# Kernel tuning notes

Hardware: AMD Instinct MI355X
Metric: run time of the kernel (lower is better)

## Reference

```python
import jax, jax.numpy as jnp
import numpy as np

IN, OUT, IO, CF, CS = 128, 128, 512, 512, 1024
B = 8192
TAU_IO, TAU_CF, TAU_CS = 2.0, 5.0, 70.0


def _lin(x, W, b):
    # torch nn.Linear: y = x @ W.T + b, W has shape [out, in]
    return x @ W.T + b


def setup_inputs() -> dict:
    key = jax.random.key(0)
    ks = jax.random.split(key, 24)

    def wb(i, fan_out, fan_in):
        s = 1.0 / np.sqrt(fan_in)
        W = jax.random.uniform(ks[2 * i], (fan_out, fan_in), jnp.float32, -s, s)
        b = jax.random.uniform(ks[2 * i + 1], (fan_out,), jnp.float32, -s, s)
        return W, b

    Wi2io, bi2io = wb(0, IO, IN)
    Wio2o, bio2o = wb(1, OUT, IO)
    Wio2io, bio2io = wb(2, IO, IO)
    Wio2cf, bio2cf = wb(3, CF, IO)
    Wcf2io, bcf2io = wb(4, IO, CF)
    Wcf2cs, bcf2cs = wb(5, CS, CF)
    Wcf2cf, bcf2cf = wb(6, CF, CF)
    Wcs2cf, bcs2cf = wb(7, CF, CS)
    Wcs2cs, bcs2cs = wb(8, CS, CS)

    x = jax.random.normal(ks[18], (B, IN), jnp.float32)
    io_state = jnp.zeros((B, IO), jnp.float32)
    cf_state = jnp.zeros((B, CF), jnp.float32)
    cs_state = jnp.zeros((B, CS), jnp.float32)

    return dict(
        x=x, io_state=io_state, cf_state=cf_state, cs_state=cs_state,
        Wi2io=Wi2io, bi2io=bi2io, Wio2o=Wio2o, bio2o=bio2o,
        Wio2io=Wio2io, bio2io=bio2io, Wio2cf=Wio2cf, bio2cf=bio2cf,
        Wcf2io=Wcf2io, bcf2io=bcf2io, Wcf2cs=Wcf2cs, bcf2cs=bcf2cs,
        Wcf2cf=Wcf2cf, bcf2cf=bcf2cf, Wcs2cf=Wcs2cf, bcs2cf=bcs2cf,
        Wcs2cs=Wcs2cs, bcs2cs=bcs2cs,
    )


def reference(x, io_state, cf_state, cs_state,
              Wi2io, bi2io, Wio2o, bio2o,
              Wio2io, bio2io, Wio2cf, bio2cf,
              Wcf2io, bcf2io, Wcf2cs, bcf2cs,
              Wcf2cf, bcf2cf, Wcs2cf, bcs2cf,
              Wcs2cs, bcs2cs):
    x = x.reshape(-1, IN)
    # leaky-integrated updates; all branches read the *previous* states
    io_new = jnp.tanh(
        (1.0 - 1.0 / TAU_IO) * io_state
        + (_lin(io_state, Wio2io, bio2io)
           + _lin(cf_state, Wcf2io, bcf2io)
           + _lin(x, Wi2io, bi2io)) / TAU_IO)
    cf_new = jnp.tanh(
        (1.0 - 1.0 / TAU_CF) * cf_state
        + (_lin(cf_state, Wcf2cf, bcf2cf)
           + _lin(cs_state, Wcs2cf, bcs2cf)
           + _lin(io_state, Wio2cf, bio2cf)) / TAU_CF)
    cs_new = jnp.tanh(
        (1.0 - 1.0 / TAU_CS) * cs_state
        + (_lin(cs_state, Wcs2cs, bcs2cs)
           + _lin(cf_state, Wcf2cs, bcf2cs)) / TAU_CS)
    y = jnp.tanh(_lin(io_new, Wio2o, bio2o))
    return y
```

## Files before the change

### kernel.cpp

```cpp
#include <hip/hip_runtime.h>


typedef float f32x4 __attribute__((ext_vector_type(4)));
typedef __bf16 bf16x8 __attribute__((ext_vector_type(8)));
typedef unsigned short u16x8 __attribute__((ext_vector_type(8)));
typedef unsigned short u16x4 __attribute__((ext_vector_type(4)));

__device__ __forceinline__ unsigned short f2bf(float f) {
    unsigned u = __builtin_bit_cast(unsigned, f);
    u += 0x7FFFu + ((u >> 16) & 1u);
    return (unsigned short)(u >> 16);
}

__device__ __forceinline__ int swz(int row, int kbyte) {
    return ((row << 7) + kbyte) ^ ((row & 7) << 4);
}

__global__ __launch_bounds__(256) void k_convert(
    const float* __restrict__ Wi2io, const float* __restrict__ Wio2io,
    const float* __restrict__ Wcf2io, const float* __restrict__ Wio2o,
    unsigned short* __restrict__ wcat, unsigned short* __restrict__ w2)
{
    int idx = blockIdx.x * 256 + threadIdx.x;
    if (idx < 147456) {
        int n = idx / 288;
        int k = (idx - n * 288) * 4;
        const float* s;
        if (k < 128)      s = Wi2io  + n * 128 + k;
        else if (k < 640) s = Wio2io + n * 512 + (k - 128);
        else              s = Wcf2io + n * 512 + (k - 640);
        f32x4 v = *(const f32x4*)s;
        u16x4 h;
        #pragma unroll
        for (int t = 0; t < 4; ++t) {
            float f = 0.5f * v[t];
            int kk = k + t;
            if (kk >= 128 && kk < 640 && (kk - 128) == n) f += 0.5f;
            h[t] = f2bf(f);
        }
        *(u16x4*)(wcat + n * 1152 + k) = h;
    } else if (idx < 163840) {
        int q = idx - 147456;
        int n = q >> 7;
        int k = (q & 127) * 4;
        f32x4 v = *(const f32x4*)(Wio2o + n * 512 + k);
        u16x4 h; h[0]=f2bf(v[0]); h[1]=f2bf(v[1]); h[2]=f2bf(v[2]); h[3]=f2bf(v[3]);
        *(u16x4*)(w2 + n * 512 + k) = h;
    }
}

__global__ __launch_bounds__(256, 2) void k_gemm1(
    const float* __restrict__ x, const float* __restrict__ io,
    const float* __restrict__ cf,
    const unsigned short* __restrict__ wcat,
    const float* __restrict__ b1, const float* __restrict__ b2,
    const float* __restrict__ b3,
    unsigned short* __restrict__ ionew)
{
    __shared__ __align__(16) char lds[2][24576];

    const int tid = threadIdx.x;
    const int b   = blockIdx.x;
    const int row_blk = (b & 7) + ((b >> 5) << 3);
    const int col_blk = (b >> 3) & 3;
    const int m0 = row_blk << 6;
    const int n0 = col_blk << 7;

    const int lane = tid & 63;
    const int wid  = tid >> 6;
    const int wm   = (wid >> 1) << 5;
    const int wn   = (wid & 1) << 6;
    const int lrow = lane & 15;
    const int lk2  = (lane >> 4) << 4;

    f32x4 ra[4]; u16x8 rb[4];
    f32x4 acc[2][4];
    f32x4 z = {0.f, 0.f, 0.f, 0.f};
    #pragma unroll
    for (int i = 0; i < 2; ++i)
        #pragma unroll
        for (int j = 0; j < 4; ++j) acc[i][j] = z;

#define ISSUE1(KT) do {                                                        \
        int K_ = (KT);                                                         \
        const float* sp; int st, c0;                                           \
        if (K_ < 2)       { sp = x;  st = 128; c0 = K_ << 6; }                 \
        else if (K_ < 10) { sp = io; st = 512; c0 = (K_ - 2) << 6; }           \
        else              { sp = cf; st = 512; c0 = (K_ - 10) << 6; }          \
        _Pragma("unroll")                                                      \
        for (int j = 0; j < 4; ++j) {                                          \
            int q = tid + 256 * j;                                             \
            ra[j] = *(const f32x4*)(sp + (size_t)(m0 + (q >> 4)) * st          \
                                       + c0 + ((q & 15) << 2));                \
        }                                                                      \
        const unsigned short* wp = wcat + (K_ << 6);                           \
        _Pragma("unroll")                                                      \
        for (int j = 0; j < 4; ++j) {                                          \
            int q = tid + 256 * j;                                             \
            rb[j] = *(const u16x8*)(wp + (size_t)(n0 + (q >> 3)) * 1152        \
                                       + ((q & 7) << 3));                      \
        }                                                                      \
    } while (0)

#define WRITE1(BUF) do {                                                       \
        char* A_ = (BUF); char* B_ = (BUF) + 8192;                             \
        _Pragma("unroll")                                                      \
        for (int j = 0; j < 4; ++j) {                                          \
            int q = tid + 256 * j;                                             \
            u16x4 h;                                                           \
            h[0] = f2bf(ra[j][0]); h[1] = f2bf(ra[j][1]);                      \
            h[2] = f2bf(ra[j][2]); h[3] = f2bf(ra[j][3]);                      \
            *(u16x4*)(A_ + swz(q >> 4, (q & 15) << 3)) = h;                    \
            *(u16x8*)(B_ + swz(q >> 3, (q & 7) << 4)) = rb[j];                 \
        }                                                                      \
    } while (0)

#define COMPUTE1(BUF) do {                                                     \
        const char* A_ = (BUF); const char* B_ = (BUF) + 8192;                 \
        _Pragma("unroll")                                                      \
        for (int ks = 0; ks < 2; ++ks) {                                       \
            int kb = ks * 64 + lk2;                                            \
            bf16x8 af[2], bfr[4];                                              \
            _Pragma("unroll")                                                  \
            for (int mi = 0; mi < 2; ++mi)                                     \
                af[mi] = *(const bf16x8*)(A_ + swz(wm + mi * 16 + lrow, kb));  \
            _Pragma("unroll")                                                  \
            for (int nj = 0; nj < 4; ++nj)                                     \
                bfr[nj] = *(const bf16x8*)(B_ + swz(wn + nj * 16 + lrow, kb)); \
            _Pragma("unroll")                                                  \
            for (int mi = 0; mi < 2; ++mi)                                     \
                _Pragma("unroll")                                              \
                for (int nj = 0; nj < 4; ++nj)                                 \
                    acc[mi][nj] = __builtin_amdgcn_mfma_f32_16x16x32_bf16(     \
                        af[mi], bfr[nj], acc[mi][nj], 0, 0, 0);                \
        }                                                                      \
    } while (0)

    ISSUE1(0);
    WRITE1(lds[0]);
    __syncthreads();
    int cur = 0;
    for (int kt = 0; kt < 18; ++kt) {
        if (kt < 17) ISSUE1(kt + 1);
        COMPUTE1(lds[cur]);
        if (kt < 17) WRITE1(lds[cur ^ 1]);
        __syncthreads();
        cur ^= 1;
    }

    #pragma unroll
    for (int nj = 0; nj < 4; ++nj) {
        int gn = n0 + wn + nj * 16 + lrow;
        float bb = 0.5f * (b1[gn] + b2[gn] + b3[gn]);
        #pragma unroll
        for (int mi = 0; mi < 2; ++mi) {
            #pragma unroll
            for (int r = 0; r < 4; ++r) {
                int gm = m0 + wm + mi * 16 + ((lane >> 4) << 2) + r;
                ionew[(size_t)gm * 512 + gn] = f2bf(tanhf(acc[mi][nj][r] + bb));
            }
        }
    }
#undef ISSUE1
#undef WRITE1
#undef COMPUTE1
}

__global__ __launch_bounds__(128, 2) void k_gemm2(
    const unsigned short* __restrict__ ionew,
    const unsigned short* __restrict__ w2,
    const float* __restrict__ b_io2o,
    float* __restrict__ out)
{
    __shared__ __align__(16) char lds[2][12288];

    const int tid = threadIdx.x;
    const int b   = blockIdx.x;
    const int r2 = 2 * (b & 7) + ((b >> 3) & 1) + ((b >> 5) << 4);
    const int c2 = (b >> 4) & 1;
    const int m0 = r2 << 5;
    const int n0 = c2 << 6;

    const int lane = tid & 63;
    const int wid  = tid >> 6;
    const int wm   = wid << 4;
    const int lrow = lane & 15;
    const int lk2  = (lane >> 4) << 4;

    u16x8 ra[2], rb[4];
    f32x4 acc[4];
    f32x4 z = {0.f, 0.f, 0.f, 0.f};
    #pragma unroll
    for (int j = 0; j < 4; ++j) acc[j] = z;

#define ISSUE2(KT) do {                                                        \
        const unsigned short* ap = ionew + ((KT) << 6);                        \
        _Pragma("unroll")                                                      \
        for (int j = 0; j < 2; ++j) {                                          \
            int q = tid + 128 * j;                                             \
            ra[j] = *(const u16x8*)(ap + (size_t)(m0 + (q >> 3)) * 512         \
                                       + ((q & 7) << 3));                      \
        }                                                                      \
        const unsigned short* bp = w2 + ((KT) << 6);                           \
        _Pragma("unroll")                                                      \
        for (int j = 0; j < 4; ++j) {                                          \
            int q = tid + 128 * j;                                             \
            rb[j] = *(const u16x8*)(bp + (size_t)(n0 + (q >> 3)) * 512         \
                                       + ((q & 7) << 3));                      \
        }                                                                      \
    } while (0)

#define WRITE2(BUF) do {                                                       \
        char* A_ = (BUF); char* B_ = (BUF) + 4096;                             \
        _Pragma("unroll")                                                      \
        for (int j = 0; j < 2; ++j) {                                          \
            int q = tid + 128 * j;                                             \
            *(u16x8*)(A_ + swz(q >> 3, (q & 7) << 4)) = ra[j];                 \
        }                                                                      \
        _Pragma("unroll")                                                      \
        for (int j = 0; j < 4; ++j) {                                          \
            int q = tid + 128 * j;                                             \
            *(u16x8*)(B_ + swz(q >> 3, (q & 7) << 4)) = rb[j];                 \
        }                                                                      \
    } while (0)

#define COMPUTE2(BUF) do {                                                     \
        const char* A_ = (BUF); const char* B_ = (BUF) + 4096;                 \
        _Pragma("unroll")                                                      \
        for (int ks = 0; ks < 2; ++ks) {                                       \
            int kb = ks * 64 + lk2;                                            \
            bf16x8 af = *(const bf16x8*)(A_ + swz(wm + lrow, kb));             \
            _Pragma("unroll")                                                  \
            for (int nj = 0; nj < 4; ++nj) {                                   \
                bf16x8 bfr = *(const bf16x8*)(B_ + swz(nj * 16 + lrow, kb));   \
                acc[nj] = __builtin_amdgcn_mfma_f32_16x16x32_bf16(             \
                    af, bfr, acc[nj], 0, 0, 0);                                \
            }                                                                  \
        }                                                                      \
    } while (0)

    ISSUE2(0);
    WRITE2(lds[0]);
    __syncthreads();
    int cur = 0;
    for (int kt = 0; kt < 8; ++kt) {
        if (kt < 7) ISSUE2(kt + 1);
        COMPUTE2(lds[cur]);
        if (kt < 7) WRITE2(lds[cur ^ 1]);
        __syncthreads();
        cur ^= 1;
    }

    #pragma unroll
    for (int nj = 0; nj < 4; ++nj) {
        int col  = n0 + nj * 16 + lrow;
        float bb = b_io2o[col];
        #pragma unroll
        for (int r = 0; r < 4; ++r) {
            int gm = m0 + wm + ((lane >> 4) << 2) + r;
            out[(size_t)gm * 128 + col] = tanhf(acc[nj][r] + bb);
        }
    }
#undef ISSUE2
#undef WRITE2
#undef COMPUTE2
}

extern "C" void kernel_launch(void* const* d_in, const int* in_sizes, int n_in,
                              void* d_out, int out_size, void* d_ws, size_t ws_size,
                              hipStream_t stream)
{
    const float* x      = (const float*)d_in[0];
    const float* io     = (const float*)d_in[1];
    const float* cf     = (const float*)d_in[2];
    const float* Wi2io  = (const float*)d_in[4];
    const float* bi2io  = (const float*)d_in[5];
    const float* Wio2o  = (const float*)d_in[6];
    const float* bio2o  = (const float*)d_in[7];
    const float* Wio2io = (const float*)d_in[8];
    const float* bio2io = (const float*)d_in[9];
    const float* Wcf2io = (const float*)d_in[12];
    const float* bcf2io = (const float*)d_in[13];
    float* out = (float*)d_out;

    char* ws = (char*)d_ws;
    unsigned short* wcat  = (unsigned short*)ws;
    unsigned short* w2    = (unsigned short*)(ws + 1179648);
    unsigned short* ionew = (unsigned short*)(ws + 1310720);

    hipLaunchKernelGGL(k_convert, dim3(640), dim3(256), 0, stream,
                       Wi2io, Wio2io, Wcf2io, Wio2o, wcat, w2);
    hipLaunchKernelGGL(k_gemm1, dim3(512), dim3(256), 0, stream,
                       x, io, cf, wcat, bi2io, bio2io, bcf2io, ionew);
    hipLaunchKernelGGL(k_gemm2, dim3(512), dim3(128), 0, stream,
                       ionew, w2, bio2o, out);
}
```

Before: 39.46 us.

## Shrink GEMM1 tile to 64x64, deepen register prefetch, remap blocks per XCD

GEMM1 moves from 64x128 tiles to 64x64 tiles, doubling the grid to 1024 blocks and raising the occupancy hint to 4 blocks per CU with smaller LDS buffers. Both GEMMs now prefetch two K-tiles ahead using two register sets and a manually unrolled ping-pong loop. Block-to-tile mapping is changed so consecutive row panels land on the same XCD, which should improve L2 locality. The cost is that the fp32 activation A tile is loaded and converted twice as often across column blocks.

```diff
diff --git a/kernel.cpp b/kernel.cpp
--- a/kernel.cpp
+++ b/kernel.cpp
@@ -49,7 +49,7 @@
     }
 }
 
-__global__ __launch_bounds__(256, 2) void k_gemm1(
+__global__ __launch_bounds__(256, 4) void k_gemm1(
     const float* __restrict__ x, const float* __restrict__ io,
     const float* __restrict__ cf,
     const unsigned short* __restrict__ wcat,
@@ -57,31 +57,34 @@
     const float* __restrict__ b3,
     unsigned short* __restrict__ ionew)
 {
-    __shared__ __align__(16) char lds[2][24576];
+    __shared__ __align__(16) char lds[2][16384];
 
     const int tid = threadIdx.x;
     const int b   = blockIdx.x;
-    const int row_blk = (b & 7) + ((b >> 5) << 3);
-    const int col_blk = (b >> 3) & 3;
-    const int m0 = row_blk << 6;
-    const int n0 = col_blk << 7;
+    const int xcd   = b & 7;
+    const int idx   = b >> 3;
+    const int panel = (xcd << 4) | (idx & 15);
+    const int colb  = idx >> 4;
+    const int m0 = panel << 6;
+    const int n0 = colb << 6;
 
     const int lane = tid & 63;
     const int wid  = tid >> 6;
     const int wm   = (wid >> 1) << 5;
-    const int wn   = (wid & 1) << 6;
+    const int wn   = (wid & 1) << 5;
     const int lrow = lane & 15;
     const int lk2  = (lane >> 4) << 4;
 
-    f32x4 ra[4]; u16x8 rb[4];
-    f32x4 acc[2][4];
+    f32x4 ra0[4], ra1[4];
+    u16x8 rb0[2], rb1[2];
+    f32x4 acc[2][2];
     f32x4 z = {0.f, 0.f, 0.f, 0.f};
     #pragma unroll
     for (int i = 0; i < 2; ++i)
         #pragma unroll
-        for (int j = 0; j < 4; ++j) acc[i][j] = z;
-
-#define ISSUE1(KT) do {                                                        \
+        for (int j = 0; j < 2; ++j) acc[i][j] = z;
+
+#define ISSUE1(RA, RB, KT) do {                                                \
         int K_ = (KT);                                                         \
         const float* sp; int st, c0;                                           \
         if (K_ < 2)       { sp = x;  st = 128; c0 = K_ << 6; }                 \
@@ -90,28 +93,32 @@
         _Pragma("unroll")                                                      \
         for (int j = 0; j < 4; ++j) {                                          \
             int q = tid + 256 * j;                                             \
-            ra[j] = *(const f32x4*)(sp + (size_t)(m0 + (q >> 4)) * st          \
+            RA[j] = *(const f32x4*)(sp + (size_t)(m0 + (q >> 4)) * st          \
                                        + c0 + ((q & 15) << 2));                \
         }                                                                      \
         const unsigned short* wp = wcat + (K_ << 6);                           \
         _Pragma("unroll")                                                      \
-        for (int j = 0; j < 4; ++j) {                                          \
+        for (int j = 0; j < 2; ++j) {                                          \
             int q = tid + 256 * j;                                             \
-            rb[j] = *(const u16x8*)(wp + (size_t)(n0 + (q >> 3)) * 1152        \
+            RB[j] = *(const u16x8*)(wp + (size_t)(n0 + (q >> 3)) * 1152        \
                                        + ((q & 7) << 3));                      \
         }                                                                      \
     } while (0)
 
-#define WRITE1(BUF) do {                                                       \
+#define WRITE1(RA, RB, BUF) do {                                               \
         char* A_ = (BUF); char* B_ = (BUF) + 8192;                             \
         _Pragma("unroll")                                                      \
         for (int j = 0; j < 4; ++j) {                                          \
             int q = tid + 256 * j;                                             \
             u16x4 h;                                                           \
-            h[0] = f2bf(ra[j][0]); h[1] = f2bf(ra[j][1]);                      \
-            h[2] = f2bf(ra[j][2]); h[3] = f2bf(ra[j][3]);                      \
+            h[0] = f2bf(RA[j][0]); h[1] = f2bf(RA[j][1]);                      \
+            h[2] = f2bf(RA[j][2]); h[3] = f2bf(RA[j][3]);                      \
             *(u16x4*)(A_ + swz(q >> 4, (q & 15) << 3)) = h;                    \
-            *(u16x8*)(B_ + swz(q >> 3, (q & 7) << 4)) = rb[j];                 \
+        }                                                                      \
+        _Pragma("unroll")                                                      \
+        for (int j = 0; j < 2; ++j) {                                          \
+            int q = tid + 256 * j;                                             \
+            *(u16x8*)(B_ + swz(q >> 3, (q & 7) << 4)) = RB[j];                 \
         }                                                                      \
     } while (0)
 
@@ -120,36 +127,42 @@
         _Pragma("unroll")                                                      \
         for (int ks = 0; ks < 2; ++ks) {                                       \
             int kb = ks * 64 + lk2;                                            \
-            bf16x8 af[2], bfr[4];                                              \
+            bf16x8 af[2], bfr[2];                                              \
             _Pragma("unroll")                                                  \
             for (int mi = 0; mi < 2; ++mi)                                     \
                 af[mi] = *(const bf16x8*)(A_ + swz(wm + mi * 16 + lrow, kb));  \
             _Pragma("unroll")                                                  \
-            for (int nj = 0; nj < 4; ++nj)                                     \
+            for (int nj = 0; nj < 2; ++nj)                                     \
                 bfr[nj] = *(const bf16x8*)(B_ + swz(wn + nj * 16 + lrow, kb)); \
             _Pragma("unroll")                                                  \
             for (int mi = 0; mi < 2; ++mi)                                     \
                 _Pragma("unroll")                                              \
-                for (int nj = 0; nj < 4; ++nj)                                 \
+                for (int nj = 0; nj < 2; ++nj)                                 \
                     acc[mi][nj] = __builtin_amdgcn_mfma_f32_16x16x32_bf16(     \
                         af[mi], bfr[nj], acc[mi][nj], 0, 0, 0);                \
         }                                                                      \
     } while (0)
 
-    ISSUE1(0);
-    WRITE1(lds[0]);
+    ISSUE1(ra0, rb0, 0);
+    ISSUE1(ra1, rb1, 1);
+    WRITE1(ra0, rb0, lds[0]);
     __syncthreads();
-    int cur = 0;
-    for (int kt = 0; kt < 18; ++kt) {
-        if (kt < 17) ISSUE1(kt + 1);
-        COMPUTE1(lds[cur]);
-        if (kt < 17) WRITE1(lds[cur ^ 1]);
+
+    #pragma unroll 1
+    for (int i = 0; i < 9; ++i) {
+        int kt = 2 * i;
+        if (kt + 2 < 18) ISSUE1(ra0, rb0, kt + 2);
+        COMPUTE1(lds[0]);
+        WRITE1(ra1, rb1, lds[1]);
         __syncthreads();
-        cur ^= 1;
+        if (kt + 3 < 18) ISSUE1(ra1, rb1, kt + 3);
+        COMPUTE1(lds[1]);
+        if (kt + 2 < 18) WRITE1(ra0, rb0, lds[0]);
+        __syncthreads();
     }
 
     #pragma unroll
-    for (int nj = 0; nj < 4; ++nj) {
+    for (int nj = 0; nj < 2; ++nj) {
         int gn = n0 + wn + nj * 16 + lrow;
         float bb = 0.5f * (b1[gn] + b2[gn] + b3[gn]);
         #pragma unroll
@@ -176,8 +189,10 @@
 
     const int tid = threadIdx.x;
     const int b   = blockIdx.x;
-    const int r2 = 2 * (b & 7) + ((b >> 3) & 1) + ((b >> 5) << 4);
-    const int c2 = (b >> 4) & 1;
+    const int xcd = b & 7;
+    const int j8  = b >> 3;
+    const int r2  = (xcd << 5) | (j8 & 31);
+    const int c2  = j8 >> 5;
     const int m0 = r2 << 5;
     const int n0 = c2 << 6;
 
@@ -187,40 +202,40 @@
     const int lrow = lane & 15;
     const int lk2  = (lane >> 4) << 4;
 
-    u16x8 ra[2], rb[4];
+    u16x8 ra0[2], rb0[4], ra1[2], rb1[4];
     f32x4 acc[4];
     f32x4 z = {0.f, 0.f, 0.f, 0.f};
     #pragma unroll
     for (int j = 0; j < 4; ++j) acc[j] = z;
 
-#define ISSUE2(KT) do {                                                        \
+#define ISSUE2(RA, RB, KT) do {                                                \
         const unsigned short* ap = ionew + ((KT) << 6);                        \
         _Pragma("unroll")                                                      \
         for (int j = 0; j < 2; ++j) {                                          \
             int q = tid + 128 * j;                                             \
-            ra[j] = *(const u16x8*)(ap + (size_t)(m0 + (q >> 3)) * 512         \
+            RA[j] = *(const u16x8*)(ap + (size_t)(m0 + (q >> 3)) * 512         \
                                        + ((q & 7) << 3));                      \
         }                                                                      \
         const unsigned short* bp = w2 + ((KT) << 6);                           \
         _Pragma("unroll")                                                      \
         for (int j = 0; j < 4; ++j) {                                          \
             int q = tid + 128 * j;                                             \
-            rb[j] = *(const u16x8*)(bp + (size_t)(n0 + (q >> 3)) * 512         \
+            RB[j] = *(const u16x8*)(bp + (size_t)(n0 + (q >> 3)) * 512         \
                                        + ((q & 7) << 3));                      \
         }                                                                      \
     } while (0)
 
-#define WRITE2(BUF) do {                                                       \
+#define WRITE2(RA, RB, BUF) do {                                               \
         char* A_ = (BUF); char* B_ = (BUF) + 4096;                             \
         _Pragma("unroll")                                                      \
         for (int j = 0; j < 2; ++j) {                                          \
             int q = tid + 128 * j;                                             \
-            *(u16x8*)(A_ + swz(q >> 3, (q & 7) << 4)) = ra[j];                 \
+            *(u16x8*)(A_ + swz(q >> 3, (q & 7) << 4)) = RA[j];                 \
         }                                                                      \
         _Pragma("unroll")                                                      \
         for (int j = 0; j < 4; ++j) {                                          \
             int q = tid + 128 * j;                                             \
-            *(u16x8*)(B_ + swz(q >> 3, (q & 7) << 4)) = rb[j];                 \
+            *(u16x8*)(B_ + swz(q >> 3, (q & 7) << 4)) = RB[j];                 \
         }                                                                      \
     } while (0)
 
@@ -239,16 +254,22 @@
         }                                                                      \
     } while (0)
 
-    ISSUE2(0);
-    WRITE2(lds[0]);
+    ISSUE2(ra0, rb0, 0);
+    ISSUE2(ra1, rb1, 1);
+    WRITE2(ra0, rb0, lds[0]);
     __syncthreads();
-    int cur = 0;
-    for (int kt = 0; kt < 8; ++kt) {
-        if (kt < 7) ISSUE2(kt + 1);
-        COMPUTE2(lds[cur]);
-        if (kt < 7) WRITE2(lds[cur ^ 1]);
+
+    #pragma unroll 1
+    for (int i = 0; i < 4; ++i) {
+        int kt = 2 * i;
+        if (kt + 2 < 8) ISSUE2(ra0, rb0, kt + 2);
+        COMPUTE2(lds[0]);
+        WRITE2(ra1, rb1, lds[1]);
         __syncthreads();
-        cur ^= 1;
+        if (kt + 3 < 8) ISSUE2(ra1, rb1, kt + 3);
+        COMPUTE2(lds[1]);
+        if (kt + 2 < 8) WRITE2(ra0, rb0, lds[0]);
+        __syncthreads();
     }
 
     #pragma unroll
@@ -290,7 +311,7 @@
 
     hipLaunchKernelGGL(k_convert, dim3(640), dim3(256), 0, stream,
                        Wi2io, Wio2io, Wcf2io, Wio2o, wcat, w2);
-    hipLaunchKernelGGL(k_gemm1, dim3(512), dim3(256), 0, stream,
+    hipLaunchKernelGGL(k_gemm1, dim3(1024), dim3(256), 0, stream,
                        x, io, cf, wcat, bi2io, bio2io, bcf2io, ionew);
     hipLaunchKernelGGL(k_gemm2, dim3(512), dim3(128), 0, stream,
                        ionew, w2, bio2o, out);
```

Measured after the change: 41.41 us. +4.9%, slower.

## Fuse both GEMMs into one kernel with register-direct operand loads

Applied to the files above, without the earlier changes.

Merges the io_new GEMM and the output GEMM into one kernel. Each 512-thread block owns 32 rows and all 512 io columns, and keeps the io_new tile in LDS as bf16 instead of writing it to global memory and reading it back. The first GEMM now loads A and B fragments straight from global memory into registers, double-buffered, with no LDS staging or barriers. tanhf is replaced by an exp/reciprocal approximation. The trade-offs are a smaller grid (256 blocks), redundant weight reads per block from cache, and slightly lower tanh accuracy.

```diff
diff --git a/kernel.cpp b/kernel.cpp
--- a/kernel.cpp
+++ b/kernel.cpp
@@ -2,6 +2,7 @@
 
 
 typedef float f32x4 __attribute__((ext_vector_type(4)));
+typedef __bf16 bf16x4 __attribute__((ext_vector_type(4)));
 typedef __bf16 bf16x8 __attribute__((ext_vector_type(8)));
 typedef unsigned short u16x8 __attribute__((ext_vector_type(8)));
 typedef unsigned short u16x4 __attribute__((ext_vector_type(4)));
@@ -12,8 +13,9 @@
     return (unsigned short)(u >> 16);
 }
 
-__device__ __forceinline__ int swz(int row, int kbyte) {
-    return ((row << 7) + kbyte) ^ ((row & 7) << 4);
+__device__ __forceinline__ float tanh_fast(float x) {
+    float e = __expf(2.0f * x);
+    return 1.0f - 2.0f * __builtin_amdgcn_rcpf(e + 1.0f);
 }
 
 __global__ __launch_bounds__(256) void k_convert(
@@ -49,31 +51,32 @@
     }
 }
 
-__global__ __launch_bounds__(256, 2) void k_gemm1(
+__global__ __launch_bounds__(512, 2) void k_fused(
     const float* __restrict__ x, const float* __restrict__ io,
     const float* __restrict__ cf,
     const unsigned short* __restrict__ wcat,
+    const unsigned short* __restrict__ w2,
     const float* __restrict__ b1, const float* __restrict__ b2,
-    const float* __restrict__ b3,
-    unsigned short* __restrict__ ionew)
+    const float* __restrict__ b3, const float* __restrict__ b4,
+    float* __restrict__ out)
 {
-    __shared__ __align__(16) char lds[2][24576];
-
-    const int tid = threadIdx.x;
-    const int b   = blockIdx.x;
-    const int row_blk = (b & 7) + ((b >> 5) << 3);
-    const int col_blk = (b >> 3) & 3;
-    const int m0 = row_blk << 6;
-    const int n0 = col_blk << 7;
-
+    __shared__ __align__(16) char hlds[32 * 1024];
+
+    const int tid  = threadIdx.x;
+    const int m0   = blockIdx.x << 5;
     const int lane = tid & 63;
     const int wid  = tid >> 6;
-    const int wm   = (wid >> 1) << 5;
-    const int wn   = (wid & 1) << 6;
-    const int lrow = lane & 15;
-    const int lk2  = (lane >> 4) << 4;
-
-    f32x4 ra[4]; u16x8 rb[4];
+    const int nw   = wid << 6;
+    const int li   = lane & 15;
+    const int lk   = (lane >> 4) << 3;
+
+    int wboff[4];
+    #pragma unroll
+    for (int nj = 0; nj < 4; ++nj)
+        wboff[nj] = (nw + nj * 16 + li) * 1152 + lk;
+
+    f32x4 Ac[8], An[8];
+    u16x8 Bc[8], Bn[8];
     f32x4 acc[2][4];
     f32x4 z = {0.f, 0.f, 0.f, 0.f};
     #pragma unroll
@@ -81,189 +84,108 @@
         #pragma unroll
         for (int j = 0; j < 4; ++j) acc[i][j] = z;
 
-#define ISSUE1(KT) do {                                                        \
+#define ISSUE(A_, B_, KT) do {                                                 \
         int K_ = (KT);                                                         \
         const float* sp; int st, c0;                                           \
         if (K_ < 2)       { sp = x;  st = 128; c0 = K_ << 6; }                 \
         else if (K_ < 10) { sp = io; st = 512; c0 = (K_ - 2) << 6; }           \
         else              { sp = cf; st = 512; c0 = (K_ - 10) << 6; }          \
         _Pragma("unroll")                                                      \
-        for (int j = 0; j < 4; ++j) {                                          \
-            int q = tid + 256 * j;                                             \
-            ra[j] = *(const f32x4*)(sp + (size_t)(m0 + (q >> 4)) * st          \
-                                       + c0 + ((q & 15) << 2));                \
+        for (int mi = 0; mi < 2; ++mi) {                                       \
+            const float* rp = sp + (size_t)(m0 + mi * 16 + li) * st + c0 + lk; \
+            _Pragma("unroll")                                                  \
+            for (int ks = 0; ks < 2; ++ks) {                                   \
+                A_[mi * 4 + ks * 2 + 0] = *(const f32x4*)(rp + ks * 32);       \
+                A_[mi * 4 + ks * 2 + 1] = *(const f32x4*)(rp + ks * 32 + 4);   \
+            }                                                                  \
         }                                                                      \
-        const unsigned short* wp = wcat + (K_ << 6);                           \
         _Pragma("unroll")                                                      \
-        for (int j = 0; j < 4; ++j) {                                          \
-            int q = tid + 256 * j;                                             \
-            rb[j] = *(const u16x8*)(wp + (size_t)(n0 + (q >> 3)) * 1152        \
-                                       + ((q & 7) << 3));                      \
-        }                                                                      \
+        for (int nj = 0; nj < 4; ++nj)                                         \
+            _Pragma("unroll")                                                  \
+            for (int ks = 0; ks < 2; ++ks)                                     \
+                B_[nj * 2 + ks] = *(const u16x8*)(wcat + wboff[nj]             \
+                                                  + (K_ << 6) + ks * 32);      \
     } while (0)
 
-#define WRITE1(BUF) do {                                                       \
-        char* A_ = (BUF); char* B_ = (BUF) + 8192;                             \
-        _Pragma("unroll")                                                      \
-        for (int j = 0; j < 4; ++j) {                                          \
-            int q = tid + 256 * j;                                             \
-            u16x4 h;                                                           \
-            h[0] = f2bf(ra[j][0]); h[1] = f2bf(ra[j][1]);                      \
-            h[2] = f2bf(ra[j][2]); h[3] = f2bf(ra[j][3]);                      \
-            *(u16x4*)(A_ + swz(q >> 4, (q & 15) << 3)) = h;                    \
-            *(u16x8*)(B_ + swz(q >> 3, (q & 7) << 4)) = rb[j];                 \
-        }                                                                      \
-    } while (0)
-
-#define COMPUTE1(BUF) do {                                                     \
-        const char* A_ = (BUF); const char* B_ = (BUF) + 8192;                 \
+#define COMPUTE(A_, B_) do {                                                   \
         _Pragma("unroll")                                                      \
         for (int ks = 0; ks < 2; ++ks) {                                       \
-            int kb = ks * 64 + lk2;                                            \
-            bf16x8 af[2], bfr[4];                                              \
-            _Pragma("unroll")                                                  \
-            for (int mi = 0; mi < 2; ++mi)                                     \
-                af[mi] = *(const bf16x8*)(A_ + swz(wm + mi * 16 + lrow, kb));  \
-            _Pragma("unroll")                                                  \
-            for (int nj = 0; nj < 4; ++nj)                                     \
-                bfr[nj] = *(const bf16x8*)(B_ + swz(wn + nj * 16 + lrow, kb)); \
+            bf16x8 af[2];                                                      \
+            _Pragma("unroll")                                                  \
+            for (int mi = 0; mi < 2; ++mi) {                                   \
+                bf16x4 lo = __builtin_convertvector(A_[mi*4+ks*2+0], bf16x4);  \
+                bf16x4 hi = __builtin_convertvector(A_[mi*4+ks*2+1], bf16x4);  \
+                af[mi] = __builtin_shufflevector(lo, hi, 0,1,2,3,4,5,6,7);     \
+            }                                                                  \
             _Pragma("unroll")                                                  \
             for (int mi = 0; mi < 2; ++mi)                                     \
                 _Pragma("unroll")                                              \
                 for (int nj = 0; nj < 4; ++nj)                                 \
                     acc[mi][nj] = __builtin_amdgcn_mfma_f32_16x16x32_bf16(     \
-                        af[mi], bfr[nj], acc[mi][nj], 0, 0, 0);                \
+                        af[mi], __builtin_bit_cast(bf16x8, B_[nj*2+ks]),       \
+                        acc[mi][nj], 0, 0, 0);                                 \
         }                                                                      \
     } while (0)
 
-    ISSUE1(0);
-    WRITE1(lds[0]);
-    __syncthreads();
-    int cur = 0;
-    for (int kt = 0; kt < 18; ++kt) {
-        if (kt < 17) ISSUE1(kt + 1);
-        COMPUTE1(lds[cur]);
-        if (kt < 17) WRITE1(lds[cur ^ 1]);
-        __syncthreads();
-        cur ^= 1;
-    }
+    ISSUE(Ac, Bc, 0);
+    ISSUE(An, Bn, 1);
+    #pragma unroll 1
+    for (int i = 0; i < 9; ++i) {
+        int kt = 2 * i;
+        COMPUTE(Ac, Bc);
+        if (kt + 2 < 18) ISSUE(Ac, Bc, kt + 2);
+        COMPUTE(An, Bn);
+        if (kt + 3 < 18) ISSUE(An, Bn, kt + 3);
+    }
+#undef ISSUE
+#undef COMPUTE
 
     #pragma unroll
     for (int nj = 0; nj < 4; ++nj) {
-        int gn = n0 + wn + nj * 16 + lrow;
-        float bb = 0.5f * (b1[gn] + b2[gn] + b3[gn]);
+        int n = nw + nj * 16 + li;
+        float bb = 0.5f * (b1[n] + b2[n] + b3[n]);
         #pragma unroll
         for (int mi = 0; mi < 2; ++mi) {
             #pragma unroll
             for (int r = 0; r < 4; ++r) {
-                int gm = m0 + wm + mi * 16 + ((lane >> 4) << 2) + r;
-                ionew[(size_t)gm * 512 + gn] = f2bf(tanhf(acc[mi][nj][r] + bb));
+                int m = mi * 16 + ((lane >> 4) << 2) + r;
+                float v = tanh_fast(acc[mi][nj][r] + bb);
+                int ad = ((m << 10) + (n << 1)) ^ ((m & 7) << 4);
+                *(unsigned short*)(hlds + ad) = f2bf(v);
             }
         }
     }
-#undef ISSUE1
-#undef WRITE1
-#undef COMPUTE1
-}
-
-__global__ __launch_bounds__(128, 2) void k_gemm2(
-    const unsigned short* __restrict__ ionew,
-    const unsigned short* __restrict__ w2,
-    const float* __restrict__ b_io2o,
-    float* __restrict__ out)
-{
-    __shared__ __align__(16) char lds[2][12288];
-
-    const int tid = threadIdx.x;
-    const int b   = blockIdx.x;
-    const int r2 = 2 * (b & 7) + ((b >> 3) & 1) + ((b >> 5) << 4);
-    const int c2 = (b >> 4) & 1;
-    const int m0 = r2 << 5;
-    const int n0 = c2 << 6;
-
-    const int lane = tid & 63;
-    const int wid  = tid >> 6;
-    const int wm   = wid << 4;
-    const int lrow = lane & 15;
-    const int lk2  = (lane >> 4) << 4;
-
-    u16x8 ra[2], rb[4];
-    f32x4 acc[4];
-    f32x4 z = {0.f, 0.f, 0.f, 0.f};
-    #pragma unroll
-    for (int j = 0; j < 4; ++j) acc[j] = z;
-
-#define ISSUE2(KT) do {                                                        \
-        const unsigned short* ap = ionew + ((KT) << 6);                        \
-        _Pragma("unroll")                                                      \
-        for (int j = 0; j < 2; ++j) {                                          \
-            int q = tid + 128 * j;                                             \
-            ra[j] = *(const u16x8*)(ap + (size_t)(m0 + (q >> 3)) * 512         \
-                                       + ((q & 7) << 3));                      \
-        }                                                                      \
-        const unsigned short* bp = w2 + ((KT) << 6);                           \
-        _Pragma("unroll")                                                      \
-        for (int j = 0; j < 4; ++j) {                                          \
-            int q = tid + 128 * j;                                             \
-            rb[j] = *(const u16x8*)(bp + (size_t)(n0 + (q >> 3)) * 512         \
-                                       + ((q & 7) << 3));                      \
-        }                                                                      \
-    } while (0)
-
-#define WRITE2(BUF) do {                                                       \
-        char* A_ = (BUF); char* B_ = (BUF) + 4096;                             \
-        _Pragma("unroll")                                                      \
-        for (int j = 0; j < 2; ++j) {                                          \
-            int q = tid + 128 * j;                                             \
-            *(u16x8*)(A_ + swz(q >> 3, (q & 7) << 4)) = ra[j];                 \
-        }                                                                      \
-        _Pragma("unroll")                                                      \
-        for (int j = 0; j < 4; ++j) {                                          \
-            int q = tid + 128 * j;                                             \
-            *(u16x8*)(B_ + swz(q >> 3, (q & 7) << 4)) = rb[j];                 \
-        }                                                                      \
-    } while (0)
-
-#define COMPUTE2(BUF) do {                                                     \
-        const char* A_ = (BUF); const char* B_ = (BUF) + 4096;                 \
-        _Pragma("unroll")                                                      \
-        for (int ks = 0; ks < 2; ++ks) {                                       \
-            int kb = ks * 64 + lk2;                                            \
-            bf16x8 af = *(const bf16x8*)(A_ + swz(wm + lrow, kb));             \
-            _Pragma("unroll")                                                  \
-            for (int nj = 0; nj < 4; ++nj) {                                   \
-                bf16x8 bfr = *(const bf16x8*)(B_ + swz(nj * 16 + lrow, kb));   \
-                acc[nj] = __builtin_amdgcn_mfma_f32_16x16x32_bf16(             \
-                    af, bfr, acc[nj], 0, 0, 0);                                \
-            }                                                                  \
-        }                                                                      \
-    } while (0)
-
-    ISSUE2(0);
-    WRITE2(lds[0]);
     __syncthreads();
-    int cur = 0;
-    for (int kt = 0; kt < 8; ++kt) {
-        if (kt < 7) ISSUE2(kt + 1);
-        COMPUTE2(lds[cur]);
-        if (kt < 7) WRITE2(lds[cur ^ 1]);
-        __syncthreads();
-        cur ^= 1;
-    }
-
-    #pragma unroll
-    for (int nj = 0; nj < 4; ++nj) {
-        int col  = n0 + nj * 16 + lrow;
-        float bb = b_io2o[col];
-        #pragma unroll
-        for (int r = 0; r < 4; ++r) {
-            int gm = m0 + wm + ((lane >> 4) << 2) + r;
-            out[(size_t)gm * 128 + col] = tanhf(acc[nj][r] + bb);
+
+    const int nb = wid << 4;
+    const int w2off = (nb + li) * 512 + lk;
+    f32x4 acc2[2];
+    acc2[0] = z; acc2[1] = z;
+
+    #pragma unroll 4
+    for (int ks = 0; ks < 16; ++ks) {
+        u16x8 aw = *(const u16x8*)(w2 + w2off + ks * 32);
+        #pragma unroll
+        for (int mf = 0; mf < 2; ++mf) {
+            int m = mf * 16 + li;
+            int ad = ((m << 10) + ((ks * 32 + lk) << 1)) ^ ((m & 7) << 4);
+            bf16x8 bw = *(const bf16x8*)(hlds + ad);
+            acc2[mf] = __builtin_amdgcn_mfma_f32_16x16x32_bf16(
+                __builtin_bit_cast(bf16x8, aw), bw, acc2[mf], 0, 0, 0);
         }
     }
-#undef ISSUE2
-#undef WRITE2
-#undef COMPUTE2
+
+    const int gnc = nb + ((lane >> 4) << 2);
+    f32x4 bb4 = *(const f32x4*)(b4 + gnc);
+    #pragma unroll
+    for (int mf = 0; mf < 2; ++mf) {
+        int gm = m0 + mf * 16 + li;
+        f32x4 o;
+        #pragma unroll
+        for (int r = 0; r < 4; ++r)
+            o[r] = tanh_fast(acc2[mf][r] + bb4[r]);
+        *(f32x4*)(out + (size_t)gm * 128 + gnc) = o;
+    }
 }
 
 extern "C" void kernel_launch(void* const* d_in, const int* in_sizes, int n_in,
@@ -284,14 +206,11 @@
     float* out = (float*)d_out;
 
     char* ws = (char*)d_ws;
-    unsigned short* wcat  = (unsigned short*)ws;
-    unsigned short* w2    = (unsigned short*)(ws + 1179648);
-    unsigned short* ionew = (unsigned short*)(ws + 1310720);
+    unsigned short* wcat = (unsigned short*)ws;
+    unsigned short* w2   = (unsigned short*)(ws + 1179648);
 
     hipLaunchKernelGGL(k_convert, dim3(640), dim3(256), 0, stream,
                        Wi2io, Wio2io, Wcf2io, Wio2o, wcat, w2);
-    hipLaunchKernelGGL(k_gemm1, dim3(512), dim3(256), 0, stream,
-                       x, io, cf, wcat, bi2io, bio2io, bcf2io, ionew);
-    hipLaunchKernelGGL(k_gemm2, dim3(512), dim3(128), 0, stream,
-                       ionew, w2, bio2o, out);
-}
+    hipLaunchKernelGGL(k_fused, dim3(256), dim3(512), 0, stream,
+                       x, io, cf, wcat, w2, bi2io, bio2io, bcf2io, bio2o, out);
+}
```

New measurement: 80.38 us. 104% more time.
